# Optimization experiments

Hardware: AMD Instinct MI355X
Metric: run time of the kernel (lower is better)

## Reference

```python
import jax, jax.numpy as jnp
import numpy as np

DIM = 64
NH = 4
WS = 8                      # window_size
OR = 0.5                    # overlap_ratio
OWS = int(WS * OR) + WS     # 12, overlap window size
PAD = int(WS * OR) // 2     # 2, gap padding
HEAD = DIM // NH            # 16
SCALE = HEAD ** -0.5


def _rpi():
    # relative position index, HAT-style OCA: query window WSxWS vs extended window OWSxOWS
    ws, wse = WS, OWS
    co = np.stack(np.meshgrid(np.arange(ws), np.arange(ws), indexing='ij')).reshape(2, -1)      # 2, ws*ws
    ce = np.stack(np.meshgrid(np.arange(wse), np.arange(wse), indexing='ij')).reshape(2, -1)    # 2, wse*wse
    rel = (ce[:, None, :] - co[:, :, None]).transpose(1, 2, 0).astype(np.int64)                 # ws*ws, wse*wse, 2
    rel += ws - 1                                   # shift to start from 0
    rel[:, :, 0] *= ws + wse - 1
    return jnp.asarray(rel.sum(-1).reshape(-1))     # (ws*ws * wse*wse,)


def setup_inputs() -> dict:
    key = jax.random.key(0)
    ks = jax.random.split(key, 5)
    B, C, H, W = 4, DIM, 256, 256
    return {
        'x': jax.random.normal(ks[0], (B, C, H, W), jnp.float32),
        'qkv_w': jax.random.normal(ks[1], (3 * C, C), jnp.float32) * 0.05,
        'qkv_b': jnp.zeros((3 * C,), jnp.float32),
        'rpb_table': jax.random.normal(ks[2], ((WS + OWS - 1) ** 2, NH), jnp.float32) * 0.02,
        'proj_w': jax.random.normal(ks[3], (C, C), jnp.float32) * 0.05,
        'proj_b': jnp.zeros((C,), jnp.float32),
    }


def reference(x, qkv_w, qkv_b, rpb_table, proj_w, proj_b):
    B, C, H, W = x.shape
    nWh, nWw = H // WS, W // WS
    nW = nWh * nWw
    Nq, No = WS * WS, OWS * OWS

    # 1x1 conv qkv
    qkv = jnp.einsum('bchw,oc->bohw', x, qkv_w) + qkv_b[None, :, None, None]
    q, kv = qkv[:, :C], qkv[:, C:]

    # q window partition: (B*nW, C, Nq), windows row-major (h then w), pixels row-major within window
    qw = q.reshape(B, C, nWh, WS, nWw, WS).transpose(0, 2, 4, 1, 3, 5).reshape(B * nW, C, Nq)

    # overlapping unfold of kv (im2col gather), stride WS, kernel OWS, pad PAD
    kvp = jnp.pad(kv, ((0, 0), (0, 0), (PAD, PAD), (PAD, PAD)))
    r = (jnp.arange(nWh) * WS)[:, None] + jnp.arange(OWS)[None, :]   # (nWh, OWS)
    c = (jnp.arange(nWw) * WS)[:, None] + jnp.arange(OWS)[None, :]   # (nWw, OWS)
    patches = kvp[:, :, r[:, None, :, None], c[None, :, None, :]]    # (B, 2C, nWh, nWw, OWS, OWS)
    patches = patches.transpose(0, 2, 3, 1, 4, 5).reshape(B * nW, 2, C, No)
    kw, vw = patches[:, 0], patches[:, 1]                            # (B*nW, C, No)

    # relative position bias: (1, NH, Nq, No)
    bias = rpb_table[_rpi()].reshape(Nq, No, NH).transpose(2, 0, 1)[None]

    qh = qw.reshape(-1, NH, HEAD, Nq)
    kh = kw.reshape(-1, NH, HEAD, No)
    vh = vw.reshape(-1, NH, HEAD, No)
    attn = jnp.einsum('bhdq,bhdk->bhqk', qh, kh) * SCALE + bias
    attn = jax.nn.softmax(attn, axis=-1)
    o = jnp.einsum('bhqk,bhdk->bhdq', attn, vh).reshape(-1, C, Nq)   # (B*nW, C, Nq)

    # output projection over channels
    o = jnp.einsum('bcn,oc->bon', o, proj_w) + proj_b[None, :, None]

    # window reverse -> (B, C, H, W)
    y = o.reshape(B, nWh, nWw, C, WS, WS).transpose(0, 3, 1, 4, 2, 5).reshape(B, C, H, W)
    return y
```

## Files before the change

### kernel.cpp

```cpp
#include <hip/hip_runtime.h>

typedef unsigned short u16;
typedef unsigned int   u32;
typedef unsigned long long u64;
typedef short bf16x8 __attribute__((ext_vector_type(8)));
typedef float f32x4  __attribute__((ext_vector_type(4)));

#define MFMA(a,b,c) __builtin_amdgcn_mfma_f32_16x16x32_bf16((a),(b),(c),0,0,0)

#if __has_builtin(__builtin_amdgcn_exp2f)
#define EXP2F(x) __builtin_amdgcn_exp2f(x)
#else
#define EXP2F(x) exp2f(x)
#endif
#if __has_builtin(__builtin_amdgcn_rcpf)
#define RCPF(x) __builtin_amdgcn_rcpf(x)
#else
#define RCPF(x) (1.0f/(x))
#endif

__device__ __forceinline__ u32 cvt_pk(float lo, float hi) {
  u32 r;
  asm("v_cvt_pk_bf16_f32 %0, %1, %2" : "=v"(r) : "v"(lo), "v"(hi));
  return r;
}
union FragU { u32 u[4]; bf16x8 v; };
__device__ __forceinline__ bf16x8 frag2(u32 a, u32 b) {
  FragU x; x.u[0] = a; x.u[1] = b; x.u[2] = 0; x.u[3] = 0; return x.v;
}
__device__ __forceinline__ bf16x8 frag4(u32 a, u32 b, u32 c, u32 d) {
  FragU x; x.u[0] = a; x.u[1] = b; x.u[2] = c; x.u[3] = d; return x.v;
}
__device__ __forceinline__ bf16x8 wfrag(const float* p) {
  f32x4 w0 = *(const f32x4*)p;
  f32x4 w1 = *(const f32x4*)(p + 4);
  return frag4(cvt_pk(w0[0], w0[1]), cvt_pk(w0[2], w0[3]),
               cvt_pk(w1[0], w1[1]), cvt_pk(w1[2], w1[3]));
}

constexpr int K_OFF = 0;
constexpr int V_OFF = 18432;
constexpr int U_OFF = 39936;
constexpr int SMEM_BYTES = 58368;

constexpr float SC_LOG2E = 0.36067376022224085f;

__global__ __launch_bounds__(256)
void bias_expand(const float* __restrict__ rpb, float* __restrict__ bexp)
{
  int gid = blockIdx.x * 256 + threadIdx.x;
  int frag = gid >> 6, l = gid & 63;
  int hh = frag / 36, rem = frag % 36, qt = rem / 9, tk = rem % 9;
  int l15 = l & 15, lg = l >> 4;
  int q = qt * 16 + l15;
  int qy = q >> 3, qx = q & 7;
  f32x4 v;
#pragma unroll
  for (int r = 0; r < 4; ++r) {
    int p = tk * 16 + lg * 4 + r;
    int ky = p / 12, kx = p - ky * 12;
    int idx = (ky - qy + 7) * 19 + (kx - qx + 7);
    v[r] = rpb[idx * 4 + hh] * 1.4426950408889634f;
  }
  *(f32x4*)(bexp + (size_t)gid * 4) = v;
}

__global__ __launch_bounds__(512, 4)
void fused_win_attn(const float* __restrict__ x, const float* __restrict__ qkv_w,
                    const float* __restrict__ qkv_b, const float* __restrict__ proj_w,
                    const float* __restrict__ proj_b, const float* __restrict__ bexp,
                    float* __restrict__ out)
{
  __shared__ __align__(16) char Sm[SMEM_BYTES];
  const int tid = threadIdx.x;
  const int l   = tid & 63;
  const int wv  = tid >> 6;
  const int l15 = l & 15;
  const int lg  = l >> 4;
  const int h   = wv >> 1, qh = wv & 1;

  int bid = blockIdx.x;
  int win = (bid & 7) * 512 + (bid >> 3);
  const int bb = win >> 10;
  const int wl = win & 1023;
  const int oy = (wl >> 5) * 8, ox = (wl & 31) * 8;
  const int py0 = oy - 2, px0 = ox - 2;

  {
    int ch = tid >> 3, j = tid & 7;
    *(u64*)(Sm + V_OFF + ch * 336 + 256 + j * 8) = 0ull;
  }
  {
    const float* xb = x + (size_t)bb * 64 * 65536;
    int pix = tid % 144;
    int cq  = tid / 144;
#pragma unroll
    for (int it = 0; it < 5; ++it) {
      if (it < 4 || tid < 256) {
        int prow = (pix * 171) >> 11;
        int pcol = pix - prow * 12;
        int gy = py0 + prow, gx = px0 + pcol;
        float v0 = 0.f, v1 = 0.f, v2 = 0.f, v3 = 0.f;
        if (((u32)gy < 256u) & ((u32)gx < 256u)) {
          const float* p = xb + (size_t)(cq * 4) * 65536 + gy * 256 + gx;
          v0 = p[0]; v1 = p[65536]; v2 = p[131072]; v3 = p[196608];
        }
        u64 pk = (u64)cvt_pk(v0, v1) | ((u64)cvt_pk(v2, v3) << 32);
        *(u64*)(Sm + U_OFF + ((pix * 128 + cq * 8) ^ ((pix & 7) << 4))) = pk;
      }
      pix += 80; int wr = (pix >= 144); pix -= wr ? 144 : 0; cq += 3 + wr;
    }
  }
  __syncthreads();

  if (wv < 4) {
    const float* wr_ = qkv_w + (size_t)(64 + wv * 16 + l15) * 64;
    bf16x8 a0 = wfrag(wr_ + lg * 8), a1 = wfrag(wr_ + 32 + lg * 8);
    float kb[4];
#pragma unroll
    for (int r = 0; r < 4; ++r) kb[r] = qkv_b[64 + wv * 16 + lg * 4 + r];
#pragma unroll
    for (int nt = 0; nt < 9; ++nt) {
      int pix = nt * 16 + l15;
      int swz = (pix & 7) << 4;
      bf16x8 b0 = *(const bf16x8*)(Sm + U_OFF + ((pix * 128 + lg * 16) ^ swz));
      bf16x8 b1 = *(const bf16x8*)(Sm + U_OFF + ((pix * 128 + 64 + lg * 16) ^ swz));
      f32x4 acc = {0.f, 0.f, 0.f, 0.f};
      acc = MFMA(a0, b0, acc);
      acc = MFMA(a1, b1, acc);
      u64 pk = (u64)cvt_pk(acc[0] + kb[0], acc[1] + kb[1]) |
               ((u64)cvt_pk(acc[2] + kb[2], acc[3] + kb[3]) << 32);
      *(u64*)(Sm + K_OFF + ((pix * 128 + wv * 32 + lg * 8) ^ swz)) = pk;
    }
  } else {
    int vt = wv - 4;
    const float* wr_ = qkv_w + (size_t)(128 + vt * 16 + l15) * 64;
    bf16x8 bw0 = wfrag(wr_ + lg * 8), bw1 = wfrag(wr_ + 32 + lg * 8);
    float vb = qkv_b[128 + vt * 16 + l15];
#pragma unroll
    for (int nt = 0; nt < 9; ++nt) {
      int pr = nt * 16 + l15;
      int swz = (pr & 7) << 4;
      bf16x8 a0 = *(const bf16x8*)(Sm + U_OFF + ((pr * 128 + lg * 16) ^ swz));
      bf16x8 a1 = *(const bf16x8*)(Sm + U_OFF + ((pr * 128 + 64 + lg * 16) ^ swz));
      f32x4 acc = {0.f, 0.f, 0.f, 0.f};
      acc = MFMA(a0, bw0, acc);
      acc = MFMA(a1, bw1, acc);
      int colb = (nt >> 1) * 64 + lg * 16 + (nt & 1) * 8;
      u64 pk = (u64)cvt_pk(acc[0] + vb, acc[1] + vb) |
               ((u64)cvt_pk(acc[2] + vb, acc[3] + vb) << 32);
      *(u64*)(Sm + V_OFF + (vt * 16 + l15) * 336 + colb) = pk;
    }
  }
  u32 qf[2][2];
  {
    const float* wq = qkv_w + (size_t)(h * 16 + l15) * 64;
    bf16x8 qa0 = wfrag(wq + lg * 8), qa1 = wfrag(wq + 32 + lg * 8);
    float qsb[4];
#pragma unroll
    for (int r = 0; r < 4; ++r) qsb[r] = qkv_b[h * 16 + lg * 4 + r] * SC_LOG2E;
#pragma unroll
    for (int t = 0; t < 2; ++t) {
      int q = (qh * 2 + t) * 16 + l15;
      int pix = ((q >> 3) + 2) * 12 + (q & 7) + 2;
      int swz = (pix & 7) << 4;
      bf16x8 b0 = *(const bf16x8*)(Sm + U_OFF + ((pix * 128 + lg * 16) ^ swz));
      bf16x8 b1 = *(const bf16x8*)(Sm + U_OFF + ((pix * 128 + 64 + lg * 16) ^ swz));
      f32x4 acc = {0.f, 0.f, 0.f, 0.f};
      acc = MFMA(qa0, b0, acc);
      acc = MFMA(qa1, b1, acc);
      qf[t][0] = cvt_pk(acc[0] * SC_LOG2E + qsb[0], acc[1] * SC_LOG2E + qsb[1]);
      qf[t][1] = cvt_pk(acc[2] * SC_LOG2E + qsb[2], acc[3] * SC_LOG2E + qsb[3]);
    }
  }
  __syncthreads();

  const int kcol = h * 32 + lg * 8;
#pragma unroll
  for (int half = 0; half < 2; ++half) {
    const bf16x8 bq = frag2(qf[half][0], qf[half][1]);
    f32x4 s[9];
#pragma unroll
    for (int tk = 0; tk < 9; ++tk) {
      int p = tk * 16 + l15;
      u64 kk = *(const u64*)(Sm + K_OFF + ((p * 128 + kcol) ^ ((p & 7) << 4)));
      f32x4 z = {0.f, 0.f, 0.f, 0.f};
      s[tk] = MFMA(frag2((u32)kk, (u32)(kk >> 32)), bq, z);
    }
    const int qt = qh * 2 + half;
    const float* bp_ = bexp + ((size_t)((h * 4 + qt) * 9) * 64 + l) * 4;
#pragma unroll
    for (int tk = 0; tk < 9; ++tk) {
      f32x4 bv = *(const f32x4*)(bp_ + tk * 256);
#pragma unroll
      for (int r = 0; r < 4; ++r) s[tk][r] += bv[r];
    }
    float mx = s[0][0];
#pragma unroll
    for (int tk = 0; tk < 9; ++tk)
#pragma unroll
      for (int r = 0; r < 4; ++r) mx = fmaxf(mx, s[tk][r]);
    mx = fmaxf(mx, __shfl_xor(mx, 16));
    mx = fmaxf(mx, __shfl_xor(mx, 32));
    float sum = 0.f;
#pragma unroll
    for (int tk = 0; tk < 9; ++tk)
#pragma unroll
      for (int r = 0; r < 4; ++r) {
        float pv = EXP2F(s[tk][r] - mx);
        s[tk][r] = pv;
        sum += pv;
      }
    sum += __shfl_xor(sum, 16);
    sum += __shfl_xor(sum, 32);
    float rs = RCPF(sum);
    u32 pk[9][2];
#pragma unroll
    for (int tk = 0; tk < 9; ++tk) {
      pk[tk][0] = cvt_pk(s[tk][0], s[tk][1]);
      pk[tk][1] = cvt_pk(s[tk][2], s[tk][3]);
    }
    f32x4 o = {0.f, 0.f, 0.f, 0.f};
#pragma unroll
    for (int s5 = 0; s5 < 5; ++s5) {
      bf16x8 av = *(const bf16x8*)(Sm + V_OFF + (h * 16 + l15) * 336 + s5 * 64 + lg * 16);
      bf16x8 bp = (s5 < 4) ? frag4(pk[2*s5][0], pk[2*s5][1], pk[2*s5+1][0], pk[2*s5+1][1])
                           : frag2(pk[8][0], pk[8][1]);
      o = MFMA(av, bp, o);
    }
    int q = (qh * 2 + half) * 16 + l15;
    u64 pko = (u64)cvt_pk(o[0] * rs, o[1] * rs) |
              ((u64)cvt_pk(o[2] * rs, o[3] * rs) << 32);
    *(u64*)(Sm + U_OFF + ((q * 128 + kcol) ^ ((q & 7) << 4))) = pko;
  }
  __syncthreads();

  {
    int mt = wv & 3;
    int nb = (wv >> 2) * 2;
    int q = mt * 16 + l15, swz = (q & 7) << 4;
    bf16x8 aa0 = *(const bf16x8*)(Sm + U_OFF + ((q * 128 + lg * 16) ^ swz));
    bf16x8 aa1 = *(const bf16x8*)(Sm + U_OFF + ((q * 128 + 64 + lg * 16) ^ swz));
    int qrow = mt * 16 + lg * 4;
    int gy = oy + (qrow >> 3), gx = ox + (qrow & 7);
#pragma unroll
    for (int nn = 0; nn < 2; ++nn) {
      int ntile = nb + nn;
      const float* pw = proj_w + (size_t)(ntile * 16 + l15) * 64;
      bf16x8 b0 = wfrag(pw + lg * 8), b1 = wfrag(pw + 32 + lg * 8);
      f32x4 acc = {0.f, 0.f, 0.f, 0.f};
      acc = MFMA(aa0, b0, acc);
      acc = MFMA(aa1, b1, acc);
      float pb = proj_b[ntile * 16 + l15];
      f32x4 st = {acc[0] + pb, acc[1] + pb, acc[2] + pb, acc[3] + pb};
      float* yp = out + (((size_t)bb * 64 + ntile * 16 + l15) * 256 + gy) * 256 + gx;
      *(f32x4*)yp = st;
    }
  }
}

extern "C" void kernel_launch(void* const* d_in, const int* in_sizes, int n_in,
                              void* d_out, int out_size, void* d_ws, size_t ws_size,
                              hipStream_t stream) {
  const float* x      = (const float*)d_in[0];
  const float* qkv_w  = (const float*)d_in[1];
  const float* qkv_b  = (const float*)d_in[2];
  const float* rpb    = (const float*)d_in[3];
  const float* proj_w = (const float*)d_in[4];
  const float* proj_b = (const float*)d_in[5];
  float* out  = (float*)d_out;
  float* bexp = (float*)d_ws;

  bias_expand<<<36, 256, 0, stream>>>(rpb, bexp);
  fused_win_attn<<<4096, 512, 0, stream>>>(x, qkv_w, qkv_b, proj_w, proj_b, bexp, out);
}
```

Measured before the change: 125.5 us.

## Alias LDS regions to shrink shared memory and raise occupancy

Drops the separate input staging region so the K, input-tile and attention-output buffers all share the same LDS bytes, cutting per-block shared memory from about 57 KB to about 39 KB. K/V projection results and attention outputs are held in registers across extra __syncthreads barriers before being written into the reused region. The launch-bounds occupancy hint rises from 4 to 6 blocks per CU, and s_setprio hints plus vectorised softmax max/exp/sum are added. The cost is two more barriers per block and more register pressure under a tighter register budget.

```diff
diff --git a/kernel.cpp b/kernel.cpp
--- a/kernel.cpp
+++ b/kernel.cpp
@@ -38,10 +38,8 @@
                cvt_pk(w1[0], w1[1]), cvt_pk(w1[2], w1[3]));
 }
 
-constexpr int K_OFF = 0;
 constexpr int V_OFF = 18432;
-constexpr int U_OFF = 39936;
-constexpr int SMEM_BYTES = 58368;
+constexpr int SMEM_BYTES = 39936;
 
 constexpr float SC_LOG2E = 0.36067376022224085f;
 
@@ -65,7 +63,7 @@
   *(f32x4*)(bexp + (size_t)gid * 4) = v;
 }
 
-__global__ __launch_bounds__(512, 4)
+__global__ __launch_bounds__(512, 6)
 void fused_win_attn(const float* __restrict__ x, const float* __restrict__ qkv_w,
                     const float* __restrict__ qkv_b, const float* __restrict__ proj_w,
                     const float* __restrict__ proj_b, const float* __restrict__ bexp,
@@ -106,13 +104,14 @@
           v0 = p[0]; v1 = p[65536]; v2 = p[131072]; v3 = p[196608];
         }
         u64 pk = (u64)cvt_pk(v0, v1) | ((u64)cvt_pk(v2, v3) << 32);
-        *(u64*)(Sm + U_OFF + ((pix * 128 + cq * 8) ^ ((pix & 7) << 4))) = pk;
+        *(u64*)(Sm + ((pix * 128 + cq * 8) ^ ((pix & 7) << 4))) = pk;
       }
       pix += 80; int wr = (pix >= 144); pix -= wr ? 144 : 0; cq += 3 + wr;
     }
   }
   __syncthreads();
 
+  u64 kv[9];
   if (wv < 4) {
     const float* wr_ = qkv_w + (size_t)(64 + wv * 16 + l15) * 64;
     bf16x8 a0 = wfrag(wr_ + lg * 8), a1 = wfrag(wr_ + 32 + lg * 8);
@@ -123,14 +122,13 @@
     for (int nt = 0; nt < 9; ++nt) {
       int pix = nt * 16 + l15;
       int swz = (pix & 7) << 4;
-      bf16x8 b0 = *(const bf16x8*)(Sm + U_OFF + ((pix * 128 + lg * 16) ^ swz));
-      bf16x8 b1 = *(const bf16x8*)(Sm + U_OFF + ((pix * 128 + 64 + lg * 16) ^ swz));
+      bf16x8 b0 = *(const bf16x8*)(Sm + ((pix * 128 + lg * 16) ^ swz));
+      bf16x8 b1 = *(const bf16x8*)(Sm + ((pix * 128 + 64 + lg * 16) ^ swz));
       f32x4 acc = {0.f, 0.f, 0.f, 0.f};
       acc = MFMA(a0, b0, acc);
       acc = MFMA(a1, b1, acc);
-      u64 pk = (u64)cvt_pk(acc[0] + kb[0], acc[1] + kb[1]) |
+      kv[nt] = (u64)cvt_pk(acc[0] + kb[0], acc[1] + kb[1]) |
                ((u64)cvt_pk(acc[2] + kb[2], acc[3] + kb[3]) << 32);
-      *(u64*)(Sm + K_OFF + ((pix * 128 + wv * 32 + lg * 8) ^ swz)) = pk;
     }
   } else {
     int vt = wv - 4;
@@ -141,15 +139,13 @@
     for (int nt = 0; nt < 9; ++nt) {
       int pr = nt * 16 + l15;
       int swz = (pr & 7) << 4;
-      bf16x8 a0 = *(const bf16x8*)(Sm + U_OFF + ((pr * 128 + lg * 16) ^ swz));
-      bf16x8 a1 = *(const bf16x8*)(Sm + U_OFF + ((pr * 128 + 64 + lg * 16) ^ swz));
+      bf16x8 a0 = *(const bf16x8*)(Sm + ((pr * 128 + lg * 16) ^ swz));
+      bf16x8 a1 = *(const bf16x8*)(Sm + ((pr * 128 + 64 + lg * 16) ^ swz));
       f32x4 acc = {0.f, 0.f, 0.f, 0.f};
       acc = MFMA(a0, bw0, acc);
       acc = MFMA(a1, bw1, acc);
-      int colb = (nt >> 1) * 64 + lg * 16 + (nt & 1) * 8;
-      u64 pk = (u64)cvt_pk(acc[0] + vb, acc[1] + vb) |
+      kv[nt] = (u64)cvt_pk(acc[0] + vb, acc[1] + vb) |
                ((u64)cvt_pk(acc[2] + vb, acc[3] + vb) << 32);
-      *(u64*)(Sm + V_OFF + (vt * 16 + l15) * 336 + colb) = pk;
     }
   }
   u32 qf[2][2];
@@ -164,8 +160,8 @@
       int q = (qh * 2 + t) * 16 + l15;
       int pix = ((q >> 3) + 2) * 12 + (q & 7) + 2;
       int swz = (pix & 7) << 4;
-      bf16x8 b0 = *(const bf16x8*)(Sm + U_OFF + ((pix * 128 + lg * 16) ^ swz));
-      bf16x8 b1 = *(const bf16x8*)(Sm + U_OFF + ((pix * 128 + 64 + lg * 16) ^ swz));
+      bf16x8 b0 = *(const bf16x8*)(Sm + ((pix * 128 + lg * 16) ^ swz));
+      bf16x8 b1 = *(const bf16x8*)(Sm + ((pix * 128 + 64 + lg * 16) ^ swz));
       f32x4 acc = {0.f, 0.f, 0.f, 0.f};
       acc = MFMA(qa0, b0, acc);
       acc = MFMA(qa1, b1, acc);
@@ -175,42 +171,62 @@
   }
   __syncthreads();
 
+  if (wv < 4) {
+#pragma unroll
+    for (int nt = 0; nt < 9; ++nt) {
+      int pix = nt * 16 + l15;
+      *(u64*)(Sm + ((pix * 128 + wv * 32 + lg * 8) ^ ((pix & 7) << 4))) = kv[nt];
+    }
+  } else {
+    int vt = wv - 4;
+#pragma unroll
+    for (int nt = 0; nt < 9; ++nt) {
+      int colb = (nt >> 1) * 64 + lg * 16 + (nt & 1) * 8;
+      *(u64*)(Sm + V_OFF + (vt * 16 + l15) * 336 + colb) = kv[nt];
+    }
+  }
+  __syncthreads();
+
   const int kcol = h * 32 + lg * 8;
+  u64 po[2];
 #pragma unroll
   for (int half = 0; half < 2; ++half) {
     const bf16x8 bq = frag2(qf[half][0], qf[half][1]);
     f32x4 s[9];
+    __builtin_amdgcn_s_setprio(1);
 #pragma unroll
     for (int tk = 0; tk < 9; ++tk) {
       int p = tk * 16 + l15;
-      u64 kk = *(const u64*)(Sm + K_OFF + ((p * 128 + kcol) ^ ((p & 7) << 4)));
+      u64 kk = *(const u64*)(Sm + ((p * 128 + kcol) ^ ((p & 7) << 4)));
       f32x4 z = {0.f, 0.f, 0.f, 0.f};
       s[tk] = MFMA(frag2((u32)kk, (u32)(kk >> 32)), bq, z);
     }
+    __builtin_amdgcn_s_setprio(0);
     const int qt = qh * 2 + half;
     const float* bp_ = bexp + ((size_t)((h * 4 + qt) * 9) * 64 + l) * 4;
 #pragma unroll
     for (int tk = 0; tk < 9; ++tk) {
       f32x4 bv = *(const f32x4*)(bp_ + tk * 256);
-#pragma unroll
-      for (int r = 0; r < 4; ++r) s[tk][r] += bv[r];
-    }
-    float mx = s[0][0];
-#pragma unroll
-    for (int tk = 0; tk < 9; ++tk)
-#pragma unroll
-      for (int r = 0; r < 4; ++r) mx = fmaxf(mx, s[tk][r]);
+      s[tk] += bv;
+    }
+    f32x4 m4 = s[0];
+#pragma unroll
+    for (int tk = 1; tk < 9; ++tk) m4 = __builtin_elementwise_max(m4, s[tk]);
+    float mx = fmaxf(fmaxf(m4[0], m4[1]), fmaxf(m4[2], m4[3]));
     mx = fmaxf(mx, __shfl_xor(mx, 16));
     mx = fmaxf(mx, __shfl_xor(mx, 32));
-    float sum = 0.f;
-#pragma unroll
-    for (int tk = 0; tk < 9; ++tk)
-#pragma unroll
-      for (int r = 0; r < 4; ++r) {
-        float pv = EXP2F(s[tk][r] - mx);
-        s[tk][r] = pv;
-        sum += pv;
-      }
+    f32x4 mx4 = {mx, mx, mx, mx};
+    f32x4 sum4 = {0.f, 0.f, 0.f, 0.f};
+#pragma unroll
+    for (int tk = 0; tk < 9; ++tk) {
+      f32x4 t = s[tk] - mx4;
+      f32x4 e;
+#pragma unroll
+      for (int r = 0; r < 4; ++r) e[r] = EXP2F(t[r]);
+      s[tk] = e;
+      sum4 += e;
+    }
+    float sum = (sum4[0] + sum4[1]) + (sum4[2] + sum4[3]);
     sum += __shfl_xor(sum, 16);
     sum += __shfl_xor(sum, 32);
     float rs = RCPF(sum);
@@ -221,6 +237,7 @@
       pk[tk][1] = cvt_pk(s[tk][2], s[tk][3]);
     }
     f32x4 o = {0.f, 0.f, 0.f, 0.f};
+    __builtin_amdgcn_s_setprio(1);
 #pragma unroll
     for (int s5 = 0; s5 < 5; ++s5) {
       bf16x8 av = *(const bf16x8*)(Sm + V_OFF + (h * 16 + l15) * 336 + s5 * 64 + lg * 16);
@@ -228,10 +245,16 @@
                            : frag2(pk[8][0], pk[8][1]);
       o = MFMA(av, bp, o);
     }
+    __builtin_amdgcn_s_setprio(0);
+    po[half] = (u64)cvt_pk(o[0] * rs, o[1] * rs) |
+               ((u64)cvt_pk(o[2] * rs, o[3] * rs) << 32);
+  }
+  __syncthreads();
+
+#pragma unroll
+  for (int half = 0; half < 2; ++half) {
     int q = (qh * 2 + half) * 16 + l15;
-    u64 pko = (u64)cvt_pk(o[0] * rs, o[1] * rs) |
-              ((u64)cvt_pk(o[2] * rs, o[3] * rs) << 32);
-    *(u64*)(Sm + U_OFF + ((q * 128 + kcol) ^ ((q & 7) << 4))) = pko;
+    *(u64*)(Sm + ((q * 128 + kcol) ^ ((q & 7) << 4))) = po[half];
   }
   __syncthreads();
 
@@ -239,8 +262,8 @@
     int mt = wv & 3;
     int nb = (wv >> 2) * 2;
     int q = mt * 16 + l15, swz = (q & 7) << 4;
-    bf16x8 aa0 = *(const bf16x8*)(Sm + U_OFF + ((q * 128 + lg * 16) ^ swz));
-    bf16x8 aa1 = *(const bf16x8*)(Sm + U_OFF + ((q * 128 + 64 + lg * 16) ^ swz));
+    bf16x8 aa0 = *(const bf16x8*)(Sm + ((q * 128 + lg * 16) ^ swz));
+    bf16x8 aa1 = *(const bf16x8*)(Sm + ((q * 128 + 64 + lg * 16) ^ swz));
     int qrow = mt * 16 + lg * 4;
     int gy = oy + (qrow >> 3), gx = ox + (qrow & 7);
 #pragma unroll
```

Result: slower. 130.5 us (+4.1%).
